# Kernel optimization log

Measured on AMD Instinct MI355X. Metric: run time of the kernel, lower is better.

The kernel has to match this reference:

```python
import jax, jax.numpy as jnp
import numpy as np
from jax import lax

B, N, R, L = 16, 256, 24, 32
MEAN_STOP_TIME_S = 60.0
AVG_TRANSFER_WAIT_TIME_S = 300.0
SYMMETRIC_ROUTES = True
INF = jnp.inf


def setup_inputs() -> dict:
    key = jax.random.key(0)
    k1, k2, k3 = jax.random.split(key, 3)
    drive_times = jax.random.uniform(k1, (B, N, N), jnp.float32) * 1000.0 + 30.0
    demand = jax.random.uniform(k2, (B, N, N), jnp.float32) * 10.0
    demand = demand * (1.0 - jnp.eye(N, dtype=jnp.float32))  # no self-demand
    batch_routes = jax.random.randint(k3, (B, R, L), 0, N, dtype=jnp.int32)
    return {"drive_times": drive_times, "demand": demand, "batch_routes": batch_routes}


def _route_edges_and_legs(routes, dtm):
    # routes: [B,R,L] node ids (no -1 padding in this setup); dtm: [B,N,N]
    b = jnp.arange(B)[:, None, None]
    sf, st = routes[:, :, :-1], routes[:, :, 1:]
    leg_fwd = dtm[b, sf, st] + MEAN_STOP_TIME_S            # [B,R,L-1]
    zero = jnp.zeros((B, R, 1), dtm.dtype)
    cum_f = jnp.concatenate([zero, jnp.cumsum(leg_fwd, -1)], -1)  # [B,R,L]
    tri = jnp.triu(jnp.ones((L, L), dtype=bool), 1)
    # ride time from stop position i to position j>i along the route
    t_f = jnp.where(tri, cum_f[:, :, None, :] - cum_f[:, :, :, None], INF)
    b4 = jnp.arange(B)[:, None, None, None]
    src = jnp.broadcast_to(routes[:, :, :, None], (B, R, L, L))
    dst = jnp.broadcast_to(routes[:, :, None, :], (B, R, L, L))
    edge = jnp.full((B, N, N), INF, dtm.dtype)
    edge = edge.at[b4, src, dst].min(t_f)
    leg_rev = None
    if SYMMETRIC_ROUTES:
        leg_rev = dtm[b, st, sf] + MEAN_STOP_TIME_S        # reverse-direction legs
        cum_r = jnp.concatenate([zero, jnp.cumsum(leg_rev, -1)], -1)
        t_r = jnp.where(tri, cum_r[:, :, None, :] - cum_r[:, :, :, None], INF)
        edge = edge.at[b4, dst, src].min(t_r)              # ride from s_j back to s_i
    return edge, leg_fwd, leg_rev


def _floyd_warshall(edge):
    # batched FW, also tracking hop count of shortest paths
    idx = jnp.arange(N)
    dist = edge.at[:, idx, idx].set(0.0)
    offdiag = ~jnp.eye(N, dtype=bool)
    hops = jnp.where(jnp.isfinite(dist) & offdiag, 1.0, 0.0)

    def body(carry, k):
        d, h = carry
        dc = lax.dynamic_slice_in_dim(d, k, 1, axis=2)  # [B,N,1]
        dr = lax.dynamic_slice_in_dim(d, k, 1, axis=1)  # [B,1,N]
        hc = lax.dynamic_slice_in_dim(h, k, 1, axis=2)
        hr = lax.dynamic_slice_in_dim(h, k, 1, axis=1)
        alt = dc + dr
        better = alt < d
        return (jnp.where(better, alt, d), jnp.where(better, hc + hr, h)), None

    (dist, hops), _ = lax.scan(body, (dist, hops), idx)
    return dist, hops


def reference(drive_times, demand, batch_routes):
    edge, leg_fwd, leg_rev = _route_edges_and_legs(batch_routes, drive_times)
    dist, hops = _floyd_warshall(edge)
    nopath = jnp.isinf(dist)
    path_lens = jnp.where(nopath, 0.0, hops + 1.0)  # n nodes on path (diag -> 1)
    transfers = jnp.where(path_lens == 0.0, 0.0, path_lens - 2.0)
    trip_times = jnp.where(nopath, 0.0, dist + transfers * AVG_TRANSFER_WAIT_TIME_S)
    total_demand_time = (demand * trip_times).sum((1, 2))
    total_transfers = (demand * transfers).sum((1, 2))
    unserved_demand = jnp.where(nopath, demand, 0.0).sum((1, 2))
    total_demand = demand.sum((1, 2))
    n_disconnected = (nopath & (demand > 0)).sum((1, 2))
    buckets = [jnp.where(transfers == float(ii), demand, 0.0).sum((1, 2)) for ii in range(3)]
    d_un = jnp.where(transfers > 2.0, demand, 0.0).sum((1, 2)) + unserved_demand
    trips_at_transfers = jnp.stack(buckets + [d_un], axis=1)  # [B,4]
    total_route_time = leg_fwd.sum((1, 2))
    if SYMMETRIC_ROUTES:
        total_route_time = total_route_time + leg_rev.sum((1, 2))
    return (total_demand_time, total_route_time, trips_at_transfers,
            total_demand, unserved_demand, total_transfers, trip_times,
            n_disconnected)
```

## Files before the change

kernel.cpp:

```cpp
#include <hip/hip_runtime.h>

#define BB 16
#define NL 256
#define RR 24
#define LL 32
#define NN (NL*NL)
#define BNN (BB*NN)
#define TT 64

#define O_TDT 0
#define O_RT  16
#define O_TAT 32
#define O_TD  96
#define O_UNS 112
#define O_TTR 128
#define O_TT  144
#define O_ND  1048720

#define HSC 9.3132257461547852e-10
#define H2  1073741824.0
#define HMASK 8191

#define RIDX(r, c2) (((r)<<6) + ((((c2) ^ ((r)&31)))<<1))
#define LDD(A, r, c2) (*(double2*)&A[RIDX((r),(c2))])

__global__ __launch_bounds__(1024) void k_init(double2* __restrict__ dist2, float* __restrict__ acc){
    int idx = blockIdx.x*1024 + threadIdx.x;
    double inf = __builtin_huge_val();
    double2 v = make_double2(inf, inf);
    int q = (idx*2) & (NN-1);
    int r = q % 257;
    if (r == 0)   v.x = 0.0;
    if (r == 256) v.y = 0.0;
    dist2[idx] = v;
    if (blockIdx.x == 0 && threadIdx.x < 256) acc[threadIdx.x] = 0.f;
}

__global__ void k_routes(const float* __restrict__ dtm, const int* __restrict__ routes,
                         unsigned long long* __restrict__ dist, float* __restrict__ acc){
    int br = blockIdx.x; int b = br / RR, r = br % RR;
    int lane = threadIdx.x;
    __shared__ int   s[LL];
    __shared__ float lf[LL], lr[LL], cf[LL], cr[LL];
    if (lane < LL) s[lane] = routes[(b*RR + r)*LL + lane];
    __syncthreads();
    if (lane < LL-1){
        int a0 = s[lane], a1 = s[lane+1];
        const float* dt = dtm + b*NN;
        lf[lane] = dt[a0*NL + a1] + 60.0f;
        lr[lane] = dt[a1*NL + a0] + 60.0f;
    }
    __syncthreads();
    if (lane == 0){
        float af = 0.f, ar = 0.f;
        cf[0] = 0.f; cr[0] = 0.f;
        for (int l = 0; l < LL-1; l++){
            af += lf[l]; ar += lr[l];
            cf[l+1] = af; cr[l+1] = ar;
        }
        atomicAdd(&acc[b*16 + 1], af + ar);
    }
    __syncthreads();
    for (int p = lane; p < LL*LL; p += 64){
        int i = p >> 5, j = p & 31;
        if (j > i){
            double vf = (double)(cf[j] - cf[i]) + HSC;
            double vr = (double)(cr[j] - cr[i]) + HSC;
            atomicMin(&dist[b*NN + s[i]*NL + s[j]], (unsigned long long)__double_as_longlong(vf));
            atomicMin(&dist[b*NN + s[j]*NL + s[i]], (unsigned long long)__double_as_longlong(vr));
        }
    }
}

__global__ __launch_bounds__(256, 1) void k_fw_round(
        const double* __restrict__ src, double* __restrict__ dst, int kb){
    int b  = blockIdx.y;
    int m  = blockIdx.x;
    int ti = m >> 2, tj = m & 3;
    int t  = threadIdx.x;
    int r0 = (t >> 4) << 2;
    int c2 = (t & 15) << 1;
    int c4 = (t & 15) << 2;
    __shared__ double KD[4096];
    __shared__ double BD[4096];
    const double* Kg = src + b*NN + kb*TT*(NL+1);
    const double* Bg = src + b*NN + kb*TT*NL + tj*TT;
    const double* Cg = src + b*NN + ti*TT*NL + kb*TT;
    const double* Dg = src + b*NN + ti*TT*NL + tj*TT;

    double2 c0[4][2], d0[4][2];
    #pragma unroll
    for (int i = 0; i < 4; i++){
        c0[i][0] = *(const double2*)(Cg + (r0+i)*NL + c4);
        c0[i][1] = *(const double2*)(Cg + (r0+i)*NL + c4 + 2);
        d0[i][0] = *(const double2*)(Dg + (r0+i)*NL + c4);
        d0[i][1] = *(const double2*)(Dg + (r0+i)*NL + c4 + 2);
    }

    #pragma unroll
    for (int u = 0; u < 8; u++){
        int fid = u*256 + t;
        int row = fid >> 5, cc = fid & 31;
        LDD(KD, row, cc) = *(const double2*)(Kg + row*NL + cc*2);
        LDD(BD, row, cc) = *(const double2*)(Bg + row*NL + cc*2);
    }
    __syncthreads();

    for (int skb = 0; skb < 4; skb++){
        int s0 = skb*16, sc2 = skb*8;
        if (t < 64){
            int i = t >> 2, jg = t & 3, rr = s0 + i, cb = sc2 + jg*2;
            double2 m0 = LDD(KD, rr, cb), m1 = LDD(KD, rr, cb+1);
            double md4[4] = {m0.x, m0.y, m1.x, m1.y};
            #pragma unroll
            for (int k = 0; k < 16; k++){
                double rd[4];
                #pragma unroll
                for (int c = 0; c < 4; c++) rd[c] = __shfl(md4[c], (k<<2)|jg);
                double cd = __shfl(md4[k&3], (i<<2)|(k>>2));
                #pragma unroll
                for (int c = 0; c < 4; c++) md4[c] = fmin(md4[c], cd + rd[c]);
            }
            LDD(KD, rr, cb)   = make_double2(md4[0], md4[1]);
            LDD(KD, rr, cb+1) = make_double2(md4[2], md4[3]);
        }
        __syncthreads();
        int rs_r  = s0 + (t >> 4);
        int rs_c2 = (t & 15) << 1;
        int cs_r  = t >> 2;
        int cs_c2 = sc2 + ((t & 3) << 1);
        double rs[4], cs[4], ar[16], ac[16];
        {
            double2 v0 = LDD(KD, rs_r, rs_c2), v1 = LDD(KD, rs_r, rs_c2+1);
            rs[0]=v0.x; rs[1]=v0.y; rs[2]=v1.x; rs[3]=v1.y;
            double2 w0 = LDD(KD, cs_r, cs_c2), w1 = LDD(KD, cs_r, cs_c2+1);
            cs[0]=w0.x; cs[1]=w0.y; cs[2]=w1.x; cs[3]=w1.y;
            #pragma unroll
            for (int c = 0; c < 8; c++){
                double2 av = LDD(KD, rs_r, sc2 + c);
                ar[2*c] = av.x; ar[2*c+1] = av.y;
                double2 aw = LDD(KD, cs_r, sc2 + c);
                ac[2*c] = aw.x; ac[2*c+1] = aw.y;
            }
        }
        #pragma unroll
        for (int k = 0; k < 16; k++){
            double2 b0 = LDD(KD, s0+k, rs_c2), b1 = LDD(KD, s0+k, rs_c2+1);
            rs[0] = fmin(rs[0], ar[k] + b0.x);
            rs[1] = fmin(rs[1], ar[k] + b0.y);
            rs[2] = fmin(rs[2], ar[k] + b1.x);
            rs[3] = fmin(rs[3], ar[k] + b1.y);
            double2 e0 = LDD(KD, s0+k, cs_c2), e1 = LDD(KD, s0+k, cs_c2+1);
            cs[0] = fmin(cs[0], ac[k] + e0.x);
            cs[1] = fmin(cs[1], ac[k] + e0.y);
            cs[2] = fmin(cs[2], ac[k] + e1.x);
            cs[3] = fmin(cs[3], ac[k] + e1.y);
        }
        __syncthreads();
        LDD(KD, rs_r, rs_c2)   = make_double2(rs[0], rs[1]);
        LDD(KD, rs_r, rs_c2+1) = make_double2(rs[2], rs[3]);
        LDD(KD, cs_r, cs_c2)   = make_double2(cs[0], cs[1]);
        LDD(KD, cs_r, cs_c2+1) = make_double2(cs[2], cs[3]);
        __syncthreads();
        double dd[4][4];
        #pragma unroll
        for (int i = 0; i < 4; i++){
            double2 v0 = LDD(KD, r0+i, c2), v1 = LDD(KD, r0+i, c2+1);
            dd[i][0]=v0.x; dd[i][1]=v0.y; dd[i][2]=v1.x; dd[i][3]=v1.y;
        }
        #pragma unroll
        for (int q4 = 0; q4 < 4; q4++){
            int kr = s0 + q4*4;
            double a[4][4], bm[4][4];
            #pragma unroll
            for (int i = 0; i < 4; i++){
                double2 a0 = LDD(KD, r0+i, sc2+q4*2), a1 = LDD(KD, r0+i, sc2+q4*2+1);
                a[i][0]=a0.x; a[i][1]=a0.y; a[i][2]=a1.x; a[i][3]=a1.y;
            }
            #pragma unroll
            for (int q = 0; q < 4; q++){
                double2 b0 = LDD(KD, kr+q, c2), b1 = LDD(KD, kr+q, c2+1);
                bm[q][0]=b0.x; bm[q][1]=b0.y; bm[q][2]=b1.x; bm[q][3]=b1.y;
            }
            #pragma unroll
            for (int q = 0; q < 4; q++)
            #pragma unroll
            for (int i = 0; i < 4; i++)
            #pragma unroll
            for (int j = 0; j < 4; j++)
                dd[i][j] = fmin(dd[i][j], a[i][q] + bm[q][j]);
        }
        __syncthreads();
        #pragma unroll
        for (int i = 0; i < 4; i++){
            LDD(KD, r0+i, c2)   = make_double2(dd[i][0], dd[i][1]);
            LDD(KD, r0+i, c2+1) = make_double2(dd[i][2], dd[i][3]);
        }
        __syncthreads();
    }

    double inf = __builtin_huge_val();
    double md[4][4];
    #pragma unroll
    for (int i = 0; i < 4; i++)
    #pragma unroll
    for (int j = 0; j < 4; j++) md[i][j] = inf;
    #pragma unroll 4
    for (int q4 = 0; q4 < 16; q4++){
        double a[4][4], bm[4][4];
        #pragma unroll
        for (int i = 0; i < 4; i++){
            double2 a0 = LDD(KD, r0+i, q4*2), a1 = LDD(KD, r0+i, q4*2+1);
            a[i][0]=a0.x; a[i][1]=a0.y; a[i][2]=a1.x; a[i][3]=a1.y;
        }
        int kr = q4*4;
        #pragma unroll
        for (int q = 0; q < 4; q++){
            double2 b0 = LDD(BD, kr+q, c2), b1 = LDD(BD, kr+q, c2+1);
            bm[q][0]=b0.x; bm[q][1]=b0.y; bm[q][2]=b1.x; bm[q][3]=b1.y;
        }
        #pragma unroll
        for (int q = 0; q < 4; q++)
        #pragma unroll
        for (int i = 0; i < 4; i++)
        #pragma unroll
        for (int j = 0; j < 4; j++)
            md[i][j] = fmin(md[i][j], a[i][q] + bm[q][j]);
    }
    __syncthreads();
    #pragma unroll
    for (int i = 0; i < 4; i++){
        LDD(BD, r0+i, c2)   = make_double2(md[i][0], md[i][1]);
        LDD(BD, r0+i, c2+1) = make_double2(md[i][2], md[i][3]);
        LDD(KD, r0+i, c2)   = c0[i][0];
        LDD(KD, r0+i, c2+1) = c0[i][1];
    }
    __syncthreads();

    double dd[4][4];
    #pragma unroll
    for (int i = 0; i < 4; i++){
        dd[i][0]=d0[i][0].x; dd[i][1]=d0[i][0].y; dd[i][2]=d0[i][1].x; dd[i][3]=d0[i][1].y;
    }
    #pragma unroll 4
    for (int q4 = 0; q4 < 16; q4++){
        double a[4][4], bm[4][4];
        #pragma unroll
        for (int i = 0; i < 4; i++){
            double2 a0 = LDD(KD, r0+i, q4*2), a1 = LDD(KD, r0+i, q4*2+1);
            a[i][0]=a0.x; a[i][1]=a0.y; a[i][2]=a1.x; a[i][3]=a1.y;
        }
        int kr = q4*4;
        #pragma unroll
        for (int q = 0; q < 4; q++){
            double2 b0 = LDD(BD, kr+q, c2), b1 = LDD(BD, kr+q, c2+1);
            bm[q][0]=b0.x; bm[q][1]=b0.y; bm[q][2]=b1.x; bm[q][3]=b1.y;
        }
        #pragma unroll
        for (int q = 0; q < 4; q++)
        #pragma unroll
        for (int i = 0; i < 4; i++)
        #pragma unroll
        for (int j = 0; j < 4; j++)
            dd[i][j] = fmin(dd[i][j], a[i][q] + bm[q][j]);
    }
    double* Od = dst + b*NN + ti*TT*NL + tj*TT;
    #pragma unroll
    for (int i = 0; i < 4; i++){
        *(double2*)(Od + (r0+i)*NL + c4)     = make_double2(dd[i][0], dd[i][1]);
        *(double2*)(Od + (r0+i)*NL + c4 + 2) = make_double2(dd[i][2], dd[i][3]);
    }
}

__global__ __launch_bounds__(1024) void k_epi(const double2* __restrict__ dist2,
        const float4* __restrict__ demand4, float* __restrict__ out, float* __restrict__ acc){
    int b = blockIdx.y;
    int fid = (b*NN >> 2) + blockIdx.x*1024 + threadIdx.x;
    long long q2 = (long long)fid * 2;
    double2 va = dist2[q2], vb = dist2[q2+1];
    double vs[4] = {va.x, va.y, vb.x, vb.y};
    float4 mv = demand4[fid];
    float ms[4] = {mv.x, mv.y, mv.z, mv.w};
    float s0=0,s1=0,s2=0,s3=0,s4=0,s5=0,s6=0,s7=0,s8=0;
    float tts[4];
    #pragma unroll
    for (int e = 0; e < 4; e++){
        double v = vs[e];
        bool np = !(v < 1e37);
        double vv = np ? 0.0 : v;
        int h = (int)(((long long)(vv * H2)) & (long long)HMASK);
        float d = (float)vv;
        float dm = ms[e];
        float pl = np ? 0.f : (float)(h + 1);
        float tr = (pl == 0.f) ? 0.f : pl - 2.f;
        float tt = np ? 0.f : d + tr*300.f;
        tts[e] = tt;
        s0 += dm*tt;
        s1 += dm*tr;
        s2 += np ? dm : 0.f;
        s3 += dm;
        s4 += (np && dm > 0.f) ? 1.f : 0.f;
        s5 += (tr == 0.f) ? dm : 0.f;
        s6 += (tr == 1.f) ? dm : 0.f;
        s7 += (tr == 2.f) ? dm : 0.f;
        s8 += (tr > 2.f) ? dm : 0.f;
    }
    ((float4*)(out + O_TT))[fid] = make_float4(tts[0],tts[1],tts[2],tts[3]);
    #define RED(x) { x += __shfl_down(x,32); x += __shfl_down(x,16); x += __shfl_down(x,8); \
                     x += __shfl_down(x,4);  x += __shfl_down(x,2);  x += __shfl_down(x,1); }
    RED(s0) RED(s1) RED(s2) RED(s3) RED(s4) RED(s5) RED(s6) RED(s7) RED(s8)
    __shared__ float red[16][9];
    int w = threadIdx.x >> 6;
    if ((threadIdx.x & 63) == 0){
        red[w][0]=s0; red[w][1]=s1; red[w][2]=s2; red[w][3]=s3; red[w][4]=s4;
        red[w][5]=s5; red[w][6]=s6; red[w][7]=s7; red[w][8]=s8;
    }
    __syncthreads();
    if (threadIdx.x < 9){
        float v = 0.f;
        #pragma unroll
        for (int ww = 0; ww < 16; ww++) v += red[ww][threadIdx.x];
        int slot = (threadIdx.x == 0) ? 0 : threadIdx.x + 1;
        atomicAdd(&acc[b*16 + slot], v);
    }
    __syncthreads();
    __shared__ int isLast;
    if (threadIdx.x == 0){
        unsigned prev = atomicAdd((unsigned int*)(acc + 255), 1u);
        isLast = (prev == 255u) ? 1 : 0;
    }
    __syncthreads();
    if (isLast && threadIdx.x < BB){
        int bb = threadIdx.x;
        float a[10];
        #pragma unroll
        for (int s = 0; s < 10; s++) a[s] = atomicAdd(&acc[bb*16 + s], 0.f);
        out[O_TDT + bb] = a[0];
        out[O_RT  + bb] = a[1];
        out[O_TAT + 4*bb + 0] = a[6];
        out[O_TAT + 4*bb + 1] = a[7];
        out[O_TAT + 4*bb + 2] = a[8];
        out[O_TAT + 4*bb + 3] = a[9] + a[3];
        out[O_TD  + bb] = a[4];
        out[O_UNS + bb] = a[3];
        out[O_TTR + bb] = a[2];
        out[O_ND  + bb] = a[5];
    }
}

extern "C" void kernel_launch(void* const* d_in, const int* in_sizes, int n_in,
                              void* d_out, int out_size, void* d_ws, size_t ws_size,
                              hipStream_t stream){
    (void)in_sizes; (void)n_in; (void)out_size; (void)ws_size;
    const float* dtm    = (const float*)d_in[0];
    const float* demand = (const float*)d_in[1];
    const int*   routes = (const int*)d_in[2];
    float* out   = (float*)d_out;
    double* distA = (double*)d_ws;
    double* distB = distA + BNN;
    float*  acc   = (float*)(distB + BNN);

    k_init  <<<512, 1024, 0, stream>>>((double2*)distA, acc);
    k_routes<<<BB*RR,  64, 0, stream>>>(dtm, routes, (unsigned long long*)distA, acc);
    k_fw_round<<<dim3(16,BB), 256, 0, stream>>>(distA, distB, 0);
    k_fw_round<<<dim3(16,BB), 256, 0, stream>>>(distB, distA, 1);
    k_fw_round<<<dim3(16,BB), 256, 0, stream>>>(distA, distB, 2);
    k_fw_round<<<dim3(16,BB), 256, 0, stream>>>(distB, distA, 3);
    k_epi<<<dim3(16,BB), 1024, 0, stream>>>((const double2*)distA,
                                            (const float4*)demand, out, acc);
}
```

Before: 256.5 us.

## Split FW k-loop across half-waves, fuse epilogue and drop init kernel

Each FW round block now uses 512 threads, with the two half-waves each covering half of the k range and combining their results via a cross-lane min shuffle. The separate epilogue kernel is fused into the final FW round, so the final distances are reduced directly from registers. The init kernel is replaced by a memset with a NaN pattern that fmin treats like infinity, plus diagonal zeroing inside the routes kernel. The aim is more active waves per CU and fewer launches and global passes, at the cost of extra shuffles and reliance on fmin's NaN semantics.

```diff
diff --git a/kernel.cpp b/kernel.cpp
--- a/kernel.cpp
+++ b/kernel.cpp
@@ -24,22 +24,15 @@
 #define RIDX(r, c2) (((r)<<6) + ((((c2) ^ ((r)&31)))<<1))
 #define LDD(A, r, c2) (*(double2*)&A[RIDX((r),(c2))])
 
-__global__ __launch_bounds__(1024) void k_init(double2* __restrict__ dist2, float* __restrict__ acc){
-    int idx = blockIdx.x*1024 + threadIdx.x;
-    double inf = __builtin_huge_val();
-    double2 v = make_double2(inf, inf);
-    int q = (idx*2) & (NN-1);
-    int r = q % 257;
-    if (r == 0)   v.x = 0.0;
-    if (r == 256) v.y = 0.0;
-    dist2[idx] = v;
-    if (blockIdx.x == 0 && threadIdx.x < 256) acc[threadIdx.x] = 0.f;
-}
-
 __global__ void k_routes(const float* __restrict__ dtm, const int* __restrict__ routes,
                          unsigned long long* __restrict__ dist, float* __restrict__ acc){
     int br = blockIdx.x; int b = br / RR, r = br % RR;
     int lane = threadIdx.x;
+    int gid = br*64 + lane;
+    if (gid < BB*NL){
+        int bq = gid >> 8, n = gid & 255;
+        ((double*)dist)[bq*NN + n*(NL+1)] = 0.0;
+    }
     __shared__ int   s[LL];
     __shared__ float lf[LL], lr[LL], cf[LL], cr[LL];
     if (lane < LL) s[lane] = routes[(b*RR + r)*LL + lane];
@@ -52,13 +45,13 @@
     }
     __syncthreads();
     if (lane == 0){
-        float af = 0.f, ar = 0.f;
+        float af = 0.f, ar2 = 0.f;
         cf[0] = 0.f; cr[0] = 0.f;
         for (int l = 0; l < LL-1; l++){
-            af += lf[l]; ar += lr[l];
-            cf[l+1] = af; cr[l+1] = ar;
-        }
-        atomicAdd(&acc[b*16 + 1], af + ar);
+            af += lf[l]; ar2 += lr[l];
+            cf[l+1] = af; cr[l+1] = ar2;
+        }
+        atomicAdd(&acc[b*16 + 1], af + ar2);
     }
     __syncthreads();
     for (int p = lane; p < LL*LL; p += 64){
@@ -72,35 +65,42 @@
     }
 }
 
-__global__ __launch_bounds__(256, 1) void k_fw_round(
-        const double* __restrict__ src, double* __restrict__ dst, int kb){
+template<bool FINAL>
+__global__ __launch_bounds__(512, 2) void k_fw(
+        const double* __restrict__ src, double* __restrict__ dst, int kb,
+        const float* __restrict__ demand, float* __restrict__ out,
+        float* __restrict__ acc){
     int b  = blockIdx.y;
     int m  = blockIdx.x;
     int ti = m >> 2, tj = m & 3;
     int t  = threadIdx.x;
-    int r0 = (t >> 4) << 2;
-    int c2 = (t & 15) << 1;
-    int c4 = (t & 15) << 2;
-    __shared__ double KD[4096];
-    __shared__ double BD[4096];
+    int w  = t >> 6, lane = t & 63;
+    int kh = lane >> 5, sub = lane & 31;
+    int cA = sub & 15, cB = cA + 16;
+    int r0 = w*8 + (sub >> 4)*4;
+    __shared__ __align__(16) double KD[4096];
+    __shared__ __align__(16) double BD[4096];
     const double* Kg = src + b*NN + kb*TT*(NL+1);
-    const double* Bg = src + b*NN + kb*TT*NL + tj*TT;
-    const double* Cg = src + b*NN + ti*TT*NL + kb*TT;
-    const double* Dg = src + b*NN + ti*TT*NL + tj*TT;
-
-    double2 c0[4][2], d0[4][2];
+    const double* Bg = src + b*NN + (kb*NL + tj)*TT;
+    const double* Cg = src + b*NN + (ti*NL + kb)*TT;
+    const double* Dg = src + b*NN + (ti*NL + tj)*TT;
+
+    double2 c0r[4];
+    #pragma unroll
+    for (int u = 0; u < 4; u++){
+        int fid = u*512 + t, row = fid >> 5, cc = fid & 31;
+        c0r[u] = *(const double2*)(Cg + row*NL + cc*2);
+    }
+    double2 d0a[4], d0b[4];
     #pragma unroll
     for (int i = 0; i < 4; i++){
-        c0[i][0] = *(const double2*)(Cg + (r0+i)*NL + c4);
-        c0[i][1] = *(const double2*)(Cg + (r0+i)*NL + c4 + 2);
-        d0[i][0] = *(const double2*)(Dg + (r0+i)*NL + c4);
-        d0[i][1] = *(const double2*)(Dg + (r0+i)*NL + c4 + 2);
-    }
-
-    #pragma unroll
-    for (int u = 0; u < 8; u++){
-        int fid = u*256 + t;
-        int row = fid >> 5, cc = fid & 31;
+        d0a[i] = *(const double2*)(Dg + (r0+i)*NL + 2*cA);
+        d0b[i] = *(const double2*)(Dg + (r0+i)*NL + 2*cB);
+    }
+
+    #pragma unroll
+    for (int u = 0; u < 4; u++){
+        int fid = u*512 + t, row = fid >> 5, cc = fid & 31;
         LDD(KD, row, cc) = *(const double2*)(Kg + row*NL + cc*2);
         LDD(BD, row, cc) = *(const double2*)(Bg + row*NL + cc*2);
     }
@@ -109,8 +109,8 @@
     for (int skb = 0; skb < 4; skb++){
         int s0 = skb*16, sc2 = skb*8;
         if (t < 64){
-            int i = t >> 2, jg = t & 3, rr = s0 + i, cb = sc2 + jg*2;
-            double2 m0 = LDD(KD, rr, cb), m1 = LDD(KD, rr, cb+1);
+            int i = t >> 2, jg = t & 3, rr = s0 + i, cbk = sc2 + jg*2;
+            double2 m0 = LDD(KD, rr, cbk), m1 = LDD(KD, rr, cbk+1);
             double md4[4] = {m0.x, m0.y, m1.x, m1.y};
             #pragma unroll
             for (int k = 0; k < 16; k++){
@@ -121,65 +121,54 @@
                 #pragma unroll
                 for (int c = 0; c < 4; c++) md4[c] = fmin(md4[c], cd + rd[c]);
             }
-            LDD(KD, rr, cb)   = make_double2(md4[0], md4[1]);
-            LDD(KD, rr, cb+1) = make_double2(md4[2], md4[3]);
+            LDD(KD, rr, cbk)   = make_double2(md4[0], md4[1]);
+            LDD(KD, rr, cbk+1) = make_double2(md4[2], md4[3]);
         }
         __syncthreads();
-        int rs_r  = s0 + (t >> 4);
-        int rs_c2 = (t & 15) << 1;
-        int cs_r  = t >> 2;
-        int cs_c2 = sc2 + ((t & 3) << 1);
-        double rs[4], cs[4], ar[16], ac[16];
         {
-            double2 v0 = LDD(KD, rs_r, rs_c2), v1 = LDD(KD, rs_r, rs_c2+1);
-            rs[0]=v0.x; rs[1]=v0.y; rs[2]=v1.x; rs[3]=v1.y;
-            double2 w0 = LDD(KD, cs_r, cs_c2), w1 = LDD(KD, cs_r, cs_c2+1);
-            cs[0]=w0.x; cs[1]=w0.y; cs[2]=w1.x; cs[3]=w1.y;
+            double sv[4], av[16];
+            int pr, pcA, pcB;
+            if (t < 256){ pr = s0 + (t >> 4); pcA = t & 15;            pcB = pcA + 16; }
+            else        { int t2 = t - 256; pr = t2 >> 2; pcA = sc2 + (t2 & 3); pcB = pcA + 4; }
+            double2 v0 = LDD(KD, pr, pcA), v1 = LDD(KD, pr, pcB);
+            sv[0]=v0.x; sv[1]=v0.y; sv[2]=v1.x; sv[3]=v1.y;
             #pragma unroll
             for (int c = 0; c < 8; c++){
-                double2 av = LDD(KD, rs_r, sc2 + c);
-                ar[2*c] = av.x; ar[2*c+1] = av.y;
-                double2 aw = LDD(KD, cs_r, sc2 + c);
-                ac[2*c] = aw.x; ac[2*c+1] = aw.y;
-            }
-        }
-        #pragma unroll
-        for (int k = 0; k < 16; k++){
-            double2 b0 = LDD(KD, s0+k, rs_c2), b1 = LDD(KD, s0+k, rs_c2+1);
-            rs[0] = fmin(rs[0], ar[k] + b0.x);
-            rs[1] = fmin(rs[1], ar[k] + b0.y);
-            rs[2] = fmin(rs[2], ar[k] + b1.x);
-            rs[3] = fmin(rs[3], ar[k] + b1.y);
-            double2 e0 = LDD(KD, s0+k, cs_c2), e1 = LDD(KD, s0+k, cs_c2+1);
-            cs[0] = fmin(cs[0], ac[k] + e0.x);
-            cs[1] = fmin(cs[1], ac[k] + e0.y);
-            cs[2] = fmin(cs[2], ac[k] + e1.x);
-            cs[3] = fmin(cs[3], ac[k] + e1.y);
-        }
-        __syncthreads();
-        LDD(KD, rs_r, rs_c2)   = make_double2(rs[0], rs[1]);
-        LDD(KD, rs_r, rs_c2+1) = make_double2(rs[2], rs[3]);
-        LDD(KD, cs_r, cs_c2)   = make_double2(cs[0], cs[1]);
-        LDD(KD, cs_r, cs_c2+1) = make_double2(cs[2], cs[3]);
+                double2 a2 = LDD(KD, pr, sc2 + c);
+                av[2*c] = a2.x; av[2*c+1] = a2.y;
+            }
+            #pragma unroll
+            for (int k = 0; k < 16; k++){
+                double2 b0 = LDD(KD, s0+k, pcA), b1 = LDD(KD, s0+k, pcB);
+                sv[0] = fmin(sv[0], av[k] + b0.x);
+                sv[1] = fmin(sv[1], av[k] + b0.y);
+                sv[2] = fmin(sv[2], av[k] + b1.x);
+                sv[3] = fmin(sv[3], av[k] + b1.y);
+            }
+            __syncthreads();
+            LDD(KD, pr, pcA) = make_double2(sv[0], sv[1]);
+            LDD(KD, pr, pcB) = make_double2(sv[2], sv[3]);
+        }
         __syncthreads();
         double dd[4][4];
         #pragma unroll
         for (int i = 0; i < 4; i++){
-            double2 v0 = LDD(KD, r0+i, c2), v1 = LDD(KD, r0+i, c2+1);
+            double2 v0 = LDD(KD, r0+i, cA), v1 = LDD(KD, r0+i, cB);
             dd[i][0]=v0.x; dd[i][1]=v0.y; dd[i][2]=v1.x; dd[i][3]=v1.y;
         }
         #pragma unroll
-        for (int q4 = 0; q4 < 4; q4++){
-            int kr = s0 + q4*4;
+        for (int q4 = 0; q4 < 2; q4++){
+            int kc = sc2 + kh*4 + q4*2;
+            int kr = s0 + kh*8 + q4*4;
             double a[4][4], bm[4][4];
             #pragma unroll
             for (int i = 0; i < 4; i++){
-                double2 a0 = LDD(KD, r0+i, sc2+q4*2), a1 = LDD(KD, r0+i, sc2+q4*2+1);
+                double2 a0 = LDD(KD, r0+i, kc), a1 = LDD(KD, r0+i, kc+1);
                 a[i][0]=a0.x; a[i][1]=a0.y; a[i][2]=a1.x; a[i][3]=a1.y;
             }
             #pragma unroll
             for (int q = 0; q < 4; q++){
-                double2 b0 = LDD(KD, kr+q, c2), b1 = LDD(KD, kr+q, c2+1);
+                double2 b0 = LDD(KD, kr+q, cA), b1 = LDD(KD, kr+q, cB);
                 bm[q][0]=b0.x; bm[q][1]=b0.y; bm[q][2]=b1.x; bm[q][3]=b1.y;
             }
             #pragma unroll
@@ -190,33 +179,39 @@
             for (int j = 0; j < 4; j++)
                 dd[i][j] = fmin(dd[i][j], a[i][q] + bm[q][j]);
         }
+        #pragma unroll
+        for (int i = 0; i < 4; i++)
+        #pragma unroll
+        for (int j = 0; j < 4; j++)
+            dd[i][j] = fmin(dd[i][j], __shfl_xor(dd[i][j], 32));
         __syncthreads();
         #pragma unroll
         for (int i = 0; i < 4; i++){
-            LDD(KD, r0+i, c2)   = make_double2(dd[i][0], dd[i][1]);
-            LDD(KD, r0+i, c2+1) = make_double2(dd[i][2], dd[i][3]);
+            LDD(KD, r0+i, cA) = make_double2(dd[i][0], dd[i][1]);
+            LDD(KD, r0+i, cB) = make_double2(dd[i][2], dd[i][3]);
         }
         __syncthreads();
     }
 
-    double inf = __builtin_huge_val();
+    double nanv = __longlong_as_double(0x7FF07FF07FF07FF0LL);
     double md[4][4];
     #pragma unroll
     for (int i = 0; i < 4; i++)
     #pragma unroll
-    for (int j = 0; j < 4; j++) md[i][j] = inf;
-    #pragma unroll 4
-    for (int q4 = 0; q4 < 16; q4++){
+    for (int j = 0; j < 4; j++) md[i][j] = nanv;
+    #pragma unroll 2
+    for (int q4 = 0; q4 < 8; q4++){
+        int kc = kh*16 + q4*2;
+        int kr = kh*32 + q4*4;
         double a[4][4], bm[4][4];
         #pragma unroll
         for (int i = 0; i < 4; i++){
-            double2 a0 = LDD(KD, r0+i, q4*2), a1 = LDD(KD, r0+i, q4*2+1);
+            double2 a0 = LDD(KD, r0+i, kc), a1 = LDD(KD, r0+i, kc+1);
             a[i][0]=a0.x; a[i][1]=a0.y; a[i][2]=a1.x; a[i][3]=a1.y;
         }
-        int kr = q4*4;
         #pragma unroll
         for (int q = 0; q < 4; q++){
-            double2 b0 = LDD(BD, kr+q, c2), b1 = LDD(BD, kr+q, c2+1);
+            double2 b0 = LDD(BD, kr+q, cA), b1 = LDD(BD, kr+q, cB);
             bm[q][0]=b0.x; bm[q][1]=b0.y; bm[q][2]=b1.x; bm[q][3]=b1.y;
         }
         #pragma unroll
@@ -227,33 +222,42 @@
         for (int j = 0; j < 4; j++)
             md[i][j] = fmin(md[i][j], a[i][q] + bm[q][j]);
     }
+    #pragma unroll
+    for (int i = 0; i < 4; i++)
+    #pragma unroll
+    for (int j = 0; j < 4; j++)
+        md[i][j] = fmin(md[i][j], __shfl_xor(md[i][j], 32));
     __syncthreads();
     #pragma unroll
     for (int i = 0; i < 4; i++){
-        LDD(BD, r0+i, c2)   = make_double2(md[i][0], md[i][1]);
-        LDD(BD, r0+i, c2+1) = make_double2(md[i][2], md[i][3]);
-        LDD(KD, r0+i, c2)   = c0[i][0];
-        LDD(KD, r0+i, c2+1) = c0[i][1];
+        LDD(BD, r0+i, cA) = make_double2(md[i][0], md[i][1]);
+        LDD(BD, r0+i, cB) = make_double2(md[i][2], md[i][3]);
+    }
+    #pragma unroll
+    for (int u = 0; u < 4; u++){
+        int fid = u*512 + t, row = fid >> 5, cc = fid & 31;
+        LDD(KD, row, cc) = c0r[u];
     }
     __syncthreads();
 
     double dd[4][4];
     #pragma unroll
     for (int i = 0; i < 4; i++){
-        dd[i][0]=d0[i][0].x; dd[i][1]=d0[i][0].y; dd[i][2]=d0[i][1].x; dd[i][3]=d0[i][1].y;
-    }
-    #pragma unroll 4
-    for (int q4 = 0; q4 < 16; q4++){
+        dd[i][0]=d0a[i].x; dd[i][1]=d0a[i].y; dd[i][2]=d0b[i].x; dd[i][3]=d0b[i].y;
+    }
+    #pragma unroll 2
+    for (int q4 = 0; q4 < 8; q4++){
+        int kc = kh*16 + q4*2;
+        int kr = kh*32 + q4*4;
         double a[4][4], bm[4][4];
         #pragma unroll
         for (int i = 0; i < 4; i++){
-            double2 a0 = LDD(KD, r0+i, q4*2), a1 = LDD(KD, r0+i, q4*2+1);
+            double2 a0 = LDD(KD, r0+i, kc), a1 = LDD(KD, r0+i, kc+1);
             a[i][0]=a0.x; a[i][1]=a0.y; a[i][2]=a1.x; a[i][3]=a1.y;
         }
-        int kr = q4*4;
         #pragma unroll
         for (int q = 0; q < 4; q++){
-            double2 b0 = LDD(BD, kr+q, c2), b1 = LDD(BD, kr+q, c2+1);
+            double2 b0 = LDD(BD, kr+q, cA), b1 = LDD(BD, kr+q, cB);
             bm[q][0]=b0.x; bm[q][1]=b0.y; bm[q][2]=b1.x; bm[q][3]=b1.y;
         }
         #pragma unroll
@@ -264,74 +268,89 @@
         for (int j = 0; j < 4; j++)
             dd[i][j] = fmin(dd[i][j], a[i][q] + bm[q][j]);
     }
-    double* Od = dst + b*NN + ti*TT*NL + tj*TT;
-    #pragma unroll
-    for (int i = 0; i < 4; i++){
-        *(double2*)(Od + (r0+i)*NL + c4)     = make_double2(dd[i][0], dd[i][1]);
-        *(double2*)(Od + (r0+i)*NL + c4 + 2) = make_double2(dd[i][2], dd[i][3]);
-    }
-}
-
-__global__ __launch_bounds__(1024) void k_epi(const double2* __restrict__ dist2,
-        const float4* __restrict__ demand4, float* __restrict__ out, float* __restrict__ acc){
-    int b = blockIdx.y;
-    int fid = (b*NN >> 2) + blockIdx.x*1024 + threadIdx.x;
-    long long q2 = (long long)fid * 2;
-    double2 va = dist2[q2], vb = dist2[q2+1];
-    double vs[4] = {va.x, va.y, vb.x, vb.y};
-    float4 mv = demand4[fid];
-    float ms[4] = {mv.x, mv.y, mv.z, mv.w};
-    float s0=0,s1=0,s2=0,s3=0,s4=0,s5=0,s6=0,s7=0,s8=0;
-    float tts[4];
-    #pragma unroll
-    for (int e = 0; e < 4; e++){
-        double v = vs[e];
-        bool np = !(v < 1e37);
-        double vv = np ? 0.0 : v;
-        int h = (int)(((long long)(vv * H2)) & (long long)HMASK);
-        float d = (float)vv;
-        float dm = ms[e];
-        float pl = np ? 0.f : (float)(h + 1);
-        float tr = (pl == 0.f) ? 0.f : pl - 2.f;
-        float tt = np ? 0.f : d + tr*300.f;
-        tts[e] = tt;
-        s0 += dm*tt;
-        s1 += dm*tr;
-        s2 += np ? dm : 0.f;
-        s3 += dm;
-        s4 += (np && dm > 0.f) ? 1.f : 0.f;
-        s5 += (tr == 0.f) ? dm : 0.f;
-        s6 += (tr == 1.f) ? dm : 0.f;
-        s7 += (tr == 2.f) ? dm : 0.f;
-        s8 += (tr > 2.f) ? dm : 0.f;
-    }
-    ((float4*)(out + O_TT))[fid] = make_float4(tts[0],tts[1],tts[2],tts[3]);
+    #pragma unroll
+    for (int i = 0; i < 4; i++)
+    #pragma unroll
+    for (int j = 0; j < 4; j++)
+        dd[i][j] = fmin(dd[i][j], __shfl_xor(dd[i][j], 32));
+
+    if (!FINAL){
+        if (kh == 0){
+            double* Od = dst + b*NN + (ti*NL + tj)*TT;
+            #pragma unroll
+            for (int i = 0; i < 4; i++){
+                *(double2*)(Od + (r0+i)*NL + 2*cA) = make_double2(dd[i][0], dd[i][1]);
+                *(double2*)(Od + (r0+i)*NL + 2*cB) = make_double2(dd[i][2], dd[i][3]);
+            }
+        }
+        return;
+    }
+
+    float s9[9];
+    #pragma unroll
+    for (int q = 0; q < 9; q++) s9[q] = 0.f;
+    if (kh == 0){
+        #pragma unroll
+        for (int i = 0; i < 4; i++){
+            const float* dmg = demand + b*NN + (ti*TT + r0 + i)*NL + tj*TT;
+            float* ttg = out + O_TT + b*NN + (ti*TT + r0 + i)*NL + tj*TT;
+            float2 m0 = *(const float2*)(dmg + 2*cA);
+            float2 m1 = *(const float2*)(dmg + 2*cB);
+            float dmv[4] = {m0.x, m0.y, m1.x, m1.y};
+            float tts[4];
+            #pragma unroll
+            for (int e = 0; e < 4; e++){
+                double v = dd[i][e];
+                bool np = !(v < 1e37);
+                double vv = np ? 0.0 : v;
+                int h = (int)(((long long)(vv * H2)) & (long long)HMASK);
+                float d = (float)vv;
+                float dm = dmv[e];
+                float pl = np ? 0.f : (float)(h + 1);
+                float tr = (pl == 0.f) ? 0.f : pl - 2.f;
+                float tt = np ? 0.f : d + tr*300.f;
+                tts[e] = tt;
+                s9[0] += dm*tt;
+                s9[1] += dm*tr;
+                s9[2] += np ? dm : 0.f;
+                s9[3] += dm;
+                s9[4] += (np && dm > 0.f) ? 1.f : 0.f;
+                s9[5] += (tr == 0.f) ? dm : 0.f;
+                s9[6] += (tr == 1.f) ? dm : 0.f;
+                s9[7] += (tr == 2.f) ? dm : 0.f;
+                s9[8] += (tr > 2.f) ? dm : 0.f;
+            }
+            *(float2*)(ttg + 2*cA) = make_float2(tts[0], tts[1]);
+            *(float2*)(ttg + 2*cB) = make_float2(tts[2], tts[3]);
+        }
+    }
     #define RED(x) { x += __shfl_down(x,32); x += __shfl_down(x,16); x += __shfl_down(x,8); \
                      x += __shfl_down(x,4);  x += __shfl_down(x,2);  x += __shfl_down(x,1); }
-    RED(s0) RED(s1) RED(s2) RED(s3) RED(s4) RED(s5) RED(s6) RED(s7) RED(s8)
-    __shared__ float red[16][9];
-    int w = threadIdx.x >> 6;
-    if ((threadIdx.x & 63) == 0){
-        red[w][0]=s0; red[w][1]=s1; red[w][2]=s2; red[w][3]=s3; red[w][4]=s4;
-        red[w][5]=s5; red[w][6]=s6; red[w][7]=s7; red[w][8]=s8;
-    }
-    __syncthreads();
-    if (threadIdx.x < 9){
+    #pragma unroll
+    for (int q = 0; q < 9; q++) RED(s9[q])
+    __syncthreads();
+    float* red = (float*)KD;
+    if (lane == 0){
+        #pragma unroll
+        for (int q = 0; q < 9; q++) red[w*9 + q] = s9[q];
+    }
+    __syncthreads();
+    if (t < 9){
         float v = 0.f;
         #pragma unroll
-        for (int ww = 0; ww < 16; ww++) v += red[ww][threadIdx.x];
-        int slot = (threadIdx.x == 0) ? 0 : threadIdx.x + 1;
+        for (int ww = 0; ww < 8; ww++) v += red[ww*9 + t];
+        int slot = (t == 0) ? 0 : t + 1;
         atomicAdd(&acc[b*16 + slot], v);
     }
     __syncthreads();
     __shared__ int isLast;
-    if (threadIdx.x == 0){
+    if (t == 0){
         unsigned prev = atomicAdd((unsigned int*)(acc + 255), 1u);
         isLast = (prev == 255u) ? 1 : 0;
     }
     __syncthreads();
-    if (isLast && threadIdx.x < BB){
-        int bb = threadIdx.x;
+    if (isLast && t < BB){
+        int bb = t;
         float a[10];
         #pragma unroll
         for (int s = 0; s < 10; s++) a[s] = atomicAdd(&acc[bb*16 + s], 0.f);
@@ -355,17 +374,16 @@
     const float* dtm    = (const float*)d_in[0];
     const float* demand = (const float*)d_in[1];
     const int*   routes = (const int*)d_in[2];
-    float* out   = (float*)d_out;
+    float* out = (float*)d_out;
     double* distA = (double*)d_ws;
     double* distB = distA + BNN;
     float*  acc   = (float*)(distB + BNN);
 
-    k_init  <<<512, 1024, 0, stream>>>((double2*)distA, acc);
-    k_routes<<<BB*RR,  64, 0, stream>>>(dtm, routes, (unsigned long long*)distA, acc);
-    k_fw_round<<<dim3(16,BB), 256, 0, stream>>>(distA, distB, 0);
-    k_fw_round<<<dim3(16,BB), 256, 0, stream>>>(distB, distA, 1);
-    k_fw_round<<<dim3(16,BB), 256, 0, stream>>>(distA, distB, 2);
-    k_fw_round<<<dim3(16,BB), 256, 0, stream>>>(distB, distA, 3);
-    k_epi<<<dim3(16,BB), 1024, 0, stream>>>((const double2*)distA,
-                                            (const float4*)demand, out, acc);
+    hipMemsetD32Async((hipDeviceptr_t)distA, 0x7FF07FF0u, (size_t)BNN*2, stream);
+    hipMemsetAsync(acc, 0, 256*sizeof(float), stream);
+    k_routes<<<BB*RR, 64, 0, stream>>>(dtm, routes, (unsigned long long*)distA, acc);
+    k_fw<false><<<dim3(16,BB), 512, 0, stream>>>(distA, distB, 0, nullptr, nullptr, nullptr);
+    k_fw<false><<<dim3(16,BB), 512, 0, stream>>>(distB, distA, 1, nullptr, nullptr, nullptr);
+    k_fw<false><<<dim3(16,BB), 512, 0, stream>>>(distA, distB, 2, nullptr, nullptr, nullptr);
+    k_fw<true> <<<dim3(16,BB), 512, 0, stream>>>(distB, nullptr, 3, demand, out, acc);
 }
```

New measurement: 251.6 us. Within noise of the previous version (-1.9%).
